# Kernel optimization log

Hardware: AMD Instinct MI355X
Metric: run time of the kernel (lower is better)

## Reference

```python
import jax, jax.numpy as jnp
import numpy as np

EPS = 1e-5  # BatchNorm eps (eval mode, running mean 0 / var 1)
NEG_SLOPE = 0.2


def _knn_idx(x, k):
    # x: [B,C,N] -> idx [B,N,k] (indices of k largest of negative sq dist = k nearest)
    inner = jnp.einsum('bcn,bcm->bnm', x, x)
    xx = jnp.sum(x * x, axis=1)  # [B,N]
    pd = 2.0 * inner - xx[:, :, None] - xx[:, None, :]
    return jax.lax.top_k(pd, k)[1]


def _edge_feature(x, k):
    # x: [B,C,N] -> edge features [B,2C,N,k] = concat(neighbor - center, center)
    idx = _knn_idx(x, k)                        # [B,N,k]
    xt = jnp.transpose(x, (0, 2, 1))            # [B,N,C]
    nbr = jax.vmap(lambda f, i: f[i])(xt, idx)  # [B,N,k,C] gather per batch
    ctr = jnp.broadcast_to(xt[:, :, None, :], nbr.shape)
    feat = jnp.concatenate([nbr - ctr, ctr], axis=-1)  # [B,N,k,2C]
    return jnp.transpose(feat, (0, 3, 1, 2))


def _bn(x, g, b):
    # eval-mode BatchNorm: running_mean=0, running_var=1 -> x * g/sqrt(1+eps) + b
    inv = 1.0 / np.sqrt(1.0 + EPS)
    sh = (1, -1) + (1,) * (x.ndim - 2)
    return x * (g * inv).reshape(sh) + b.reshape(sh)


def _lrelu(x):
    return jnp.where(x >= 0, x, NEG_SLOPE * x)


def _conv2d(x, w, b):  # 1x1 Conv2d: x [B,Ci,N,K], w [Ci,Co]
    return jnp.einsum('bcnk,co->bonk', x, w) + b[None, :, None, None]


def _conv1d(x, w, b):  # 1x1 Conv1d: x [B,Ci,N], w [Ci,Co]
    return jnp.einsum('bcn,co->bon', x, w) + b[None, :, None]


def setup_inputs() -> dict:
    key = jax.random.key(0)
    ks = jax.random.split(key, 24)
    B, N = 8, 4096
    rn = lambda k, sh, s=0.1: (jax.random.normal(k, sh, dtype=jnp.float32) * s)
    inp = {
        'point': jax.random.normal(ks[0], (B, 3, N), dtype=jnp.float32),
        # conv1_1: Conv2d(6,64)
        'w11': rn(ks[1], (6, 64)), 'b11': rn(ks[2], (64,)),
        'g11': jnp.ones((64,), jnp.float32), 'bb11': jnp.zeros((64,), jnp.float32),
        # conv1_2: Conv2d(6,64)
        'w12': rn(ks[3], (6, 64)), 'b12': rn(ks[4], (64,)),
        'g12': jnp.ones((64,), jnp.float32), 'bb12': jnp.zeros((64,), jnp.float32),
        # conv1_3: Conv1d(128,64)
        'w13': rn(ks[5], (128, 64)), 'b13': rn(ks[6], (64,)),
        'g13': jnp.ones((64,), jnp.float32), 'bb13': jnp.zeros((64,), jnp.float32),
        # conv1_5: Conv2d(128,64)
        'w15': rn(ks[7], (128, 64)), 'b15': rn(ks[8], (64,)),
        'g15': jnp.ones((64,), jnp.float32), 'bb15': jnp.zeros((64,), jnp.float32),
        # conv1_4: Conv1d(64,128)
        'w14': rn(ks[9], (64, 128)), 'b14': rn(ks[10], (128,)),
        'g14': jnp.ones((128,), jnp.float32), 'bb14': jnp.zeros((128,), jnp.float32),
        # fc1: Linear(128,64) + ReLU + Linear(64,3)
        'wf1': rn(ks[11], (128, 64)), 'bf1': rn(ks[12], (64,)),
        'wf2': rn(ks[13], (64, 3)), 'bf2': rn(ks[14], (3,)),
    }
    return inp


def reference(point, w11, b11, g11, bb11, w12, b12, g12, bb12,
              w13, b13, g13, bb13, w15, b15, g15, bb15,
              w14, b14, g14, bb14, wf1, bf1, wf2, bf2):
    # point: [B,3,N]
    f = _edge_feature(point, 8)                    # [B,6,N,8]
    f1 = _lrelu(_bn(_conv2d(f, w11, b11), g11, bb11)).max(axis=-1)   # [B,64,N]
    f = _edge_feature(point, 16)                   # [B,6,N,16]
    f2 = _lrelu(_bn(_conv2d(f, w12, b12), g12, bb12)).max(axis=-1)   # [B,64,N]
    f = jnp.concatenate([f1, f2], axis=1)          # [B,128,N]
    f = _lrelu(_bn(_conv1d(f, w13, b13), g13, bb13))                 # [B,64,N]
    g = _edge_feature(f, 16)                       # [B,128,N,16]
    g = _lrelu(_bn(_conv2d(g, w15, b15), g15, bb15)).max(axis=-1)    # [B,64,N]
    g = _lrelu(_bn(_conv1d(g, w14, b14), g14, bb14))                 # [B,128,N]
    feat = jnp.transpose(g, (0, 2, 1))             # [B,N,128]
    h = jax.nn.relu(feat @ wf1 + bf1) @ wf2 + bf2  # [B,N,3]
    refinepoint = h + jnp.transpose(point, (0, 2, 1))
    return feat, refinepoint
```

## Files before the change

### kernel.cpp

```cpp
#include <hip/hip_runtime.h>
#include <math.h>

#define NB 8
#define NP 4096
#define FEAT_SZ (NB * NP * 128)
#define INVBN 0.9999950000374999f
#define SPLIT 2
#define CHUNKS 32

typedef unsigned long long u64;
typedef unsigned int u32;

__device__ __forceinline__ u32 fmap(float f) {
    u32 b = __float_as_uint(f);
    return b ^ ((u32)((int)b >> 31) | 0x80000000u);
}

__device__ __forceinline__ u64 umax64(u64 a, u64 b) { return a > b ? a : b; }

__device__ __forceinline__ void kins(u64 (&v)[16], u64 key) {
    if (key <= v[15]) return;
    bool bb[16];
#pragma unroll
    for (int j = 0; j < 16; ++j) bb[j] = key > v[j];
#pragma unroll
    for (int j = 15; j >= 1; --j) v[j] = bb[j] ? (bb[j - 1] ? v[j - 1] : key) : v[j];
    if (bb[0]) v[0] = key;
}

__device__ __forceinline__ void bufpush(u64 (&v)[16], u64 &q0, u64 &q1, u64 &q2, u64 &q3,
                                        int &cnt, u64 key) {
    if (cnt < 4) {
        q0 = cnt == 0 ? key : q0;
        q1 = cnt == 1 ? key : q1;
        q2 = cnt == 2 ? key : q2;
        q3 = cnt == 3 ? key : q3;
        ++cnt;
    } else {
        kins(v, key);
    }
}

__device__ __forceinline__ void bufflush(u64 (&v)[16], u64 &q0, u64 &q1, u64 &q2, u64 &q3,
                                         int &cnt) {
    kins(v, q0); kins(v, q1); kins(v, q2); kins(v, q3);
    q0 = 0; q1 = 0; q2 = 0; q3 = 0; cnt = 0;
}

__device__ __forceinline__ void bclean(u64 (&v)[16]) {
#pragma unroll
    for (int d = 8; d; d >>= 1) {
#pragma unroll
        for (int i = 0; i < 16; ++i) {
            if ((i & d) == 0) {
                u64 a = v[i], b = v[i | d];
                bool s = a < b;
                v[i] = s ? b : a;
                v[i | d] = s ? a : b;
            }
        }
    }
}

__device__ __forceinline__ void merge_shfl(u64 (&v)[16], int off) {
    u64 o[16];
#pragma unroll
    for (int j = 0; j < 16; ++j) o[j] = __shfl_down(v[j], off);
#pragma unroll
    for (int j = 0; j < 16; ++j) {
        u64 b = o[15 - j];
        v[j] = v[j] > b ? v[j] : b;
    }
    bclean(v);
}

__device__ __forceinline__ u64 rowmax8(u64 x) {
    x = umax64(x, __shfl_xor(x, 1));
    x = umax64(x, __shfl_xor(x, 2));
    x = umax64(x, __shfl_xor(x, 4));
    return x;
}

__global__ __launch_bounds__(256) void knn_point_kernel(const float* __restrict__ point,
                                                        int* __restrict__ idxP) {
    __shared__ float4 pts[NP];
    int bt = blockIdx.x >> 7;
    int n0 = (blockIdx.x & 127) << 5;
    const float* pb = point + (size_t)bt * 3 * NP;
    for (int m = threadIdx.x; m < NP; m += 256) {
        float x = pb[m], y = pb[NP + m], z = pb[2 * NP + m];
        pts[m] = make_float4(x, y, z, fmaf(z, z, fmaf(y, y, x * x)));
    }
    __syncthreads();
    int t = threadIdx.x;
    int q = t & 7;
    float4 c = pts[n0 + (t >> 3)];
    u64 v[16];
#pragma unroll
    for (int j = 0; j < 16; ++j) v[j] = 0;
    u64 b0 = 0, b1 = 0, b2 = 0, b3 = 0;
    int cnt = 0;
    u64 th = 0;
#pragma unroll 1
    for (int o = 0; o < 8; ++o) {
#pragma unroll 4
        for (int ii = 0; ii < 64; ++ii) {
            int m = (((o << 6) + ii) << 3) + q;
            float4 p = pts[m];
            float inner = fmaf(c.z, p.z, fmaf(c.y, p.y, c.x * p.x));
            float pd = fmaf(2.0f, inner, -c.w) - p.w;
            u64 key = ((u64)fmap(pd) << 32) | (u64)(u32)~m;
            if (key > th) bufpush(v, b0, b1, b2, b3, cnt, key);
        }
        if (__any(cnt >= 3)) {
            bufflush(v, b0, b1, b2, b3, cnt);
            th = rowmax8(v[15]);
        }
    }
    bufflush(v, b0, b1, b2, b3, cnt);
    merge_shfl(v, 4);
    merge_shfl(v, 2);
    merge_shfl(v, 1);
    if (q == 0) {
        int* op = idxP + ((size_t)bt * NP + n0 + (t >> 3)) * 16;
#pragma unroll
        for (int j = 0; j < 16; ++j) op[j] = (int)~(u32)v[j];
    }
}

__global__ __launch_bounds__(256) void edge12_kernel(
    const float* __restrict__ point, const int* __restrict__ idxP,
    const float* __restrict__ w11, const float* __restrict__ b11,
    const float* __restrict__ g11, const float* __restrict__ bb11,
    const float* __restrict__ w12, const float* __restrict__ b12,
    const float* __restrict__ g12, const float* __restrict__ bb12,
    float* __restrict__ f12) {
    int lane = threadIdx.x & 63;
    int pt = blockIdx.x * 4 + (threadIdx.x >> 6);
    int bt = pt >> 12, n = pt & (NP - 1);
    const float* pb = point + (size_t)bt * 3 * NP;
    float wd1[3], wc1[3], wd2[3], wc2[3];
#pragma unroll
    for (int c = 0; c < 3; ++c) {
        wd1[c] = w11[c * 64 + lane]; wc1[c] = w11[(3 + c) * 64 + lane];
        wd2[c] = w12[c * 64 + lane]; wc2[c] = w12[(3 + c) * 64 + lane];
    }
    float s1 = g11[lane] * INVBN, sh1 = bb11[lane];
    float s2 = g12[lane] * INVBN, sh2 = bb12[lane];
    float cx = pb[n], cy = pb[NP + n], cz = pb[2 * NP + n];
    float base1 = fmaf(wc1[2], cz, fmaf(wc1[1], cy, fmaf(wc1[0], cx, b11[lane])));
    float base2 = fmaf(wc2[2], cz, fmaf(wc2[1], cy, fmaf(wc2[0], cx, b12[lane])));
    float a1 = -INFINITY, a2 = -INFINITY;
    const int* nb = idxP + (size_t)pt * 16;
#pragma unroll
    for (int j = 0; j < 16; ++j) {
        int m = nb[j];
        float ex = pb[m] - cx, ey = pb[NP + m] - cy, ez = pb[2 * NP + m] - cz;
        float y2 = fmaf(wd2[2], ez, fmaf(wd2[1], ey, fmaf(wd2[0], ex, base2)));
        float z2 = fmaf(y2, s2, sh2);
        z2 = z2 >= 0.f ? z2 : 0.2f * z2;
        a2 = fmaxf(a2, z2);
        if (j < 8) {
            float y1 = fmaf(wd1[2], ez, fmaf(wd1[1], ey, fmaf(wd1[0], ex, base1)));
            float z1 = fmaf(y1, s1, sh1);
            z1 = z1 >= 0.f ? z1 : 0.2f * z1;
            a1 = fmaxf(a1, z1);
        }
    }
    f12[((size_t)pt << 7) + lane] = a1;
    f12[((size_t)pt << 7) + 64 + lane] = a2;
}

template<int K, int O, int MODE, bool XX>
__global__ __launch_bounds__(256) void gemm_act_kernel(
        const float* __restrict__ in, const float* __restrict__ W,
        const float* __restrict__ b, const float* __restrict__ g,
        const float* __restrict__ s, float* __restrict__ outp,
        float* __restrict__ xxo) {
    __shared__ __align__(16) char smem[64 * (K + 1) * 4 + K * O * 4];
    float* A  = (float*)smem;
    float* Wl = (float*)(smem + 64 * (K + 1) * 4);
    float* Hs = (float*)smem;
    constexpr int F4R = K / 4;
#pragma unroll
    for (int i = 0; i < 64 * F4R / 256; ++i) {
        int f = threadIdx.x + i * 256;
        int pt = f / F4R, c4 = f % F4R;
        float4 v = *(const float4*)(in + ((size_t)blockIdx.x * 64 + pt) * K + c4 * 4);
        float* d = A + pt * (K + 1) + c4 * 4;
        d[0] = v.x; d[1] = v.y; d[2] = v.z; d[3] = v.w;
    }
    if constexpr (MODE == 0) {
#pragma unroll
        for (int i = 0; i < 8; ++i) {
            int f = threadIdx.x + i * 256;
            int half = f >= 1024;
            int fr = f & 1023;
            int c = fr >> 4, o4 = fr & 15;
            const float* src = half ? (W + (64 + c) * 64 + o4 * 4) : (W + c * 64 + o4 * 4);
            float4 v = *(const float4*)src;
            float* d = Wl + c * 128 + half * 64 + o4 * 4;
            d[0] = v.x; d[1] = v.y; d[2] = v.z; d[3] = v.w;
        }
    } else {
#pragma unroll
        for (int i = 0; i < K * O / 1024; ++i) {
            int f = threadIdx.x + i * 256;
            *(float4*)(Wl + f * 4) = *(const float4*)(W + f * 4);
        }
    }
    __syncthreads();
    constexpr int NO = O / 8;
    int po = threadIdx.x & 7, pp = threadIdx.x >> 3;
    int pt0 = pp * 2, o0 = po * NO;
    float acc[2][NO];
#pragma unroll
    for (int i = 0; i < NO; ++i) {
        int o = o0 + i;
        float init;
        if constexpr (MODE == 0) init = (o < 64) ? 0.f : b[o - 64];
        else init = b[o];
        acc[0][i] = init;
        acc[1][i] = init;
    }
#pragma unroll 8
    for (int kk = 0; kk < K; ++kk) {
        float a0 = A[pt0 * (K + 1) + kk];
        float a1 = A[(pt0 + 1) * (K + 1) + kk];
        float w[NO];
#pragma unroll
        for (int i4 = 0; i4 < NO / 4; ++i4) {
            float4 wv = *(const float4*)(Wl + kk * O + o0 + i4 * 4);
            w[i4 * 4 + 0] = wv.x; w[i4 * 4 + 1] = wv.y;
            w[i4 * 4 + 2] = wv.z; w[i4 * 4 + 3] = wv.w;
        }
#pragma unroll
        for (int i = 0; i < NO; ++i) {
            acc[0][i] = fmaf(a0, w[i], acc[0][i]);
            acc[1][i] = fmaf(a1, w[i], acc[1][i]);
        }
    }
    float tact[2][NO];
#pragma unroll
    for (int p = 0; p < 2; ++p) {
#pragma unroll
        for (int i = 0; i < NO; ++i) {
            int o = o0 + i;
            float a = acc[p][i];
            if constexpr (MODE == 0) {
                tact[p][i] = a;
            } else {
                float vv = fmaf(a, g[o] * INVBN, s[o]);
                tact[p][i] = vv >= 0.f ? vv : 0.2f * vv;
            }
        }
    }
#pragma unroll
    for (int p = 0; p < 2; ++p) {
        size_t rowg = (size_t)blockIdx.x * 64 + pt0 + p;
#pragma unroll
        for (int i4 = 0; i4 < NO / 4; ++i4) {
            float4 ov;
            ov.x = tact[p][i4 * 4 + 0]; ov.y = tact[p][i4 * 4 + 1];
            ov.z = tact[p][i4 * 4 + 2]; ov.w = tact[p][i4 * 4 + 3];
            *(float4*)(outp + rowg * O + o0 + i4 * 4) = ov;
        }
    }
    if constexpr (XX) {
        __syncthreads();
#pragma unroll
        for (int p = 0; p < 2; ++p)
#pragma unroll
            for (int i = 0; i < NO; ++i)
                Hs[(pt0 + p) * 65 + o0 + i] = tact[p][i];
        __syncthreads();
        if (threadIdx.x < 64) {
            float ss = 0.f;
#pragma unroll
            for (int c = 0; c < 64; ++c) {
                float hc = Hs[threadIdx.x * 65 + c];
                ss = fmaf(hc, hc, ss);
            }
            xxo[(size_t)blockIdx.x * 64 + threadIdx.x] = ss;
        }
    }
}

__global__ __launch_bounds__(256, 2) void knn_feat_kernel(const float* __restrict__ h1t,
                                                          const float* __restrict__ xxf,
                                                          u64* __restrict__ partF) {
    __shared__ __align__(16) char smem[81920];
    float* At = (float*)smem;
    float* Bt = (float*)(smem + 32768);
    u32*   Sb = (u32*)(smem + 49152);
    int seg = blockIdx.x & 1;
    int rg  = (blockIdx.x >> 1) & 31;
    int bt  = blockIdx.x >> 6;
    int n0  = rg << 7;
    int tid = threadIdx.x;
    int rp = tid >> 4;
    int cg = tid & 15;
    int cs = cg << 2;
    const float* hbase = h1t + ((size_t)bt * NP << 6);
    const float* hA = hbase + ((size_t)n0 << 6);
#pragma unroll
    for (int rep = 0; rep < 8; ++rep) {
        int row = rep * 16 + rp;
        float4 va = *(const float4*)(hA + (row << 6) + cs);
        float fv[4] = {va.x, va.y, va.z, va.w};
#pragma unroll
        for (int i = 0; i < 4; ++i) {
            int ch = cs + i;
            int rw = row ^ ((row & 32) >> 3) ^ (((ch >> 2) & 7) << 2);
            At[ch * 128 + rw] = fv[i];
        }
    }
    int m00 = seg * (CHUNKS * 64);
#pragma unroll
    for (int rep = 0; rep < 4; ++rep) {
        int col = rep * 16 + rp;
        float4 vb = *(const float4*)(hbase + ((size_t)(m00 + col) << 6) + cs);
        float fv[4] = {vb.x, vb.y, vb.z, vb.w};
#pragma unroll
        for (int i = 0; i < 4; ++i) {
            int ch = cs + i;
            int cl = col ^ ((col & 32) >> 3) ^ (((ch >> 2) & 7) << 2);
            Bt[ch * 64 + cl] = fv[i];
        }
    }
    float xa[8];
    {
        const float* xap = xxf + bt * NP + n0 + rp * 8;
        float4 t0 = *(const float4*)xap;
        float4 t1 = *(const float4*)(xap + 4);
        xa[0]=t0.x; xa[1]=t0.y; xa[2]=t0.z; xa[3]=t0.w;
        xa[4]=t1.x; xa[5]=t1.y; xa[6]=t1.z; xa[7]=t1.w;
    }
    int r = tid >> 1, h = tid & 1;
    u64 v[16];
#pragma unroll
    for (int j = 0; j < 16; ++j) v[j] = 0;
    u64 q0 = 0, q1 = 0, q2 = 0, q3 = 0;
    int cnt = 0;
    u32 th32 = 0;
    int ab0 = (rp * 8) ^ (rp & 4);
    int ab1 = (rp * 8 + 4) ^ (rp & 4);
    int cb0 = (cg * 4) ^ ((cg & 8) >> 1);
    int swQ = ((r ^ (r >> 3)) & 7) << 2;
    __syncthreads();
#pragma unroll 1
    for (int mcl = 0; mcl < CHUNKS; ++mcl) {
        int m0c = m00 + (mcl << 6);
        bool more = (mcl + 1) < CHUNKS;
        float4 nv0, nv1, nv2, nv3;
        if (more) {
            const float* hn = hbase + ((size_t)(m0c + 64) << 6);
            nv0 = *(const float4*)(hn + ((0 * 16 + rp) << 6) + cs);
            nv1 = *(const float4*)(hn + ((1 * 16 + rp) << 6) + cs);
            nv2 = *(const float4*)(hn + ((2 * 16 + rp) << 6) + cs);
            nv3 = *(const float4*)(hn + ((3 * 16 + rp) << 6) + cs);
        }
        float4 xbv = *(const float4*)(xxf + bt * NP + m0c + (cg << 2));
        float acc[8][4];
#pragma unroll
        for (int i = 0; i < 8; ++i)
#pragma unroll
            for (int j = 0; j < 4; ++j) acc[i][j] = 0.f;
#pragma unroll 1
        for (int gI = 0; gI < 16; ++gI) {
            int sw = (gI & 7) << 2;
            const float* pa0 = At + (gI << 9) + (ab0 ^ sw);
            const float* pa1 = At + (gI << 9) + (ab1 ^ sw);
            const float* pbq = Bt + (gI << 8) + (cb0 ^ sw);
#pragma unroll
            for (int u = 0; u < 4; ++u) {
                float4 a0 = *(const float4*)(pa0 + (u << 7));
                float4 a1 = *(const float4*)(pa1 + (u << 7));
                float4 bq = *(const float4*)(pbq + (u << 6));
                float av[8] = {a0.x, a0.y, a0.z, a0.w, a1.x, a1.y, a1.z, a1.w};
                float bv[4] = {bq.x, bq.y, bq.z, bq.w};
#pragma unroll
                for (int i = 0; i < 8; ++i)
#pragma unroll
                    for (int j = 0; j < 4; ++j)
                        acc[i][j] = fmaf(av[i], bv[j], acc[i][j]);
            }
        }
        float xbs[4] = {xbv.x, xbv.y, xbv.z, xbv.w};
#pragma unroll
        for (int i = 0; i < 8; ++i) {
            int row = rp * 8 + i;
            u32 k0, k1, k2, k3;
            {
                float pd;
                pd = fmaf(2.0f, acc[i][0], -xa[i]) - xbs[0]; k0 = fmap(pd);
                pd = fmaf(2.0f, acc[i][1], -xa[i]) - xbs[1]; k1 = fmap(pd);
                pd = fmaf(2.0f, acc[i][2], -xa[i]) - xbs[2]; k2 = fmap(pd);
                pd = fmaf(2.0f, acc[i][3], -xa[i]) - xbs[3]; k3 = fmap(pd);
            }
            int sq = ((row ^ (row >> 3)) & 7) << 2;
            *(uint4*)(Sb + row * 64 + ((cg << 2) ^ sq)) = make_uint4(k0, k1, k2, k3);
        }
        __syncthreads();
#pragma unroll
        for (int sI = 0; sI < 8; ++sI) {
            int c0 = h * 32 + (sI << 2);
            uint4 kq = *(const uint4*)(Sb + r * 64 + (c0 ^ swQ));
            u32 m01 = kq.x > kq.y ? kq.x : kq.y;
            u32 m23 = kq.z > kq.w ? kq.z : kq.w;
            u32 mx = m01 > m23 ? m01 : m23;
            if (mx >= th32) {
                u32 ks[4] = {kq.x, kq.y, kq.z, kq.w};
#pragma unroll
                for (int j = 0; j < 4; ++j) {
                    if (ks[j] >= th32) {
                        u64 key = ((u64)ks[j] << 32) | (u64)(u32)~(m0c + c0 + j);
                        bufpush(v, q0, q1, q2, q3, cnt, key);
                    }
                }
            }
        }
        if (more) {
            float fva[4][4] = {{nv0.x, nv0.y, nv0.z, nv0.w}, {nv1.x, nv1.y, nv1.z, nv1.w},
                               {nv2.x, nv2.y, nv2.z, nv2.w}, {nv3.x, nv3.y, nv3.z, nv3.w}};
#pragma unroll
            for (int rep = 0; rep < 4; ++rep) {
                int col = rep * 16 + rp;
#pragma unroll
                for (int i = 0; i < 4; ++i) {
                    int ch = cs + i;
                    int cl = col ^ ((col & 32) >> 3) ^ (((ch >> 2) & 7) << 2);
                    Bt[ch * 64 + cl] = fva[rep][i];
                }
            }
        }
        if (__any(cnt >= 3)) {
            bufflush(v, q0, q1, q2, q3, cnt);
            u64 m = umax64(v[15], __shfl_xor(v[15], 1));
            th32 = (u32)(m >> 32);
        }
        __syncthreads();
    }
    bufflush(v, q0, q1, q2, q3, cnt);
    merge_shfl(v, 1);
    if (h == 0) {
        u64* op = partF + (((size_t)bt * NP + n0 + r) * SPLIT + seg) * 16;
#pragma unroll
        for (int j = 0; j < 16; ++j) op[j] = v[j];
    }
}

__global__ __launch_bounds__(256) void edge5_combine_kernel(const float* __restrict__ ZC,
        const u64* __restrict__ partF,
        const float* __restrict__ g15, const float* __restrict__ bb15,
        float* __restrict__ g64t) {
    __shared__ int midx[4][16];
    int lane = threadIdx.x & 63;
    int w = threadIdx.x >> 6;
    int pt = blockIdx.x * 4 + w;
    int bt = pt >> 12;
    if (lane == 0) {
        const u64* base = partF + (size_t)pt * (SPLIT * 16);
        u64 a[16];
#pragma unroll
        for (int j = 0; j < 16; ++j) a[j] = base[j];
#pragma unroll
        for (int j = 0; j < 16; ++j) {
            u64 x = base[16 + (15 - j)];
            a[j] = a[j] > x ? a[j] : x;
        }
        bclean(a);
#pragma unroll
        for (int j = 0; j < 16; ++j) midx[w][j] = (int)~(u32)a[j];
    }
    __syncthreads();
    const float* zrow = ZC + ((size_t)pt << 7);
    float zn = zrow[lane];
    float d = zrow[64 + lane] - zn;
    float sc = g15[lane] * INVBN, sh = bb15[lane];
    const float* zb = ZC + (((size_t)bt * NP) << 7);
    float a = -INFINITY;
    float zm = zb[((size_t)midx[w][0] << 7) + lane];
#pragma unroll 1
    for (int j = 0; j < 16; ++j) {
        float zc = zm;
        if (j < 15) zm = zb[((size_t)midx[w][j + 1] << 7) + lane];
        float y = zc + d;
        float z = fmaf(y, sc, sh);
        z = z >= 0.f ? z : 0.2f * z;
        a = fmaxf(a, z);
    }
    g64t[((size_t)pt << 6) + lane] = a;
}

__global__ __launch_bounds__(256) void fc_head_kernel(const float* __restrict__ feat,
        const float* __restrict__ point,
        const float* __restrict__ wf1, const float* __restrict__ bf1,
        const float* __restrict__ wf2, const float* __restrict__ bf2,
        float* __restrict__ out) {
    __shared__ float A[64 * 129];
    __shared__ float Wl[128 * 64];
    __shared__ float wf2l[192];
    float* R = Wl;
#pragma unroll
    for (int i = 0; i < 8; ++i) {
        int f = threadIdx.x + i * 256;
        int pt = f >> 5, c4 = f & 31;
        float4 v = *(const float4*)(feat + ((size_t)blockIdx.x * 64 + pt) * 128 + c4 * 4);
        float* d = A + pt * 129 + c4 * 4;
        d[0] = v.x; d[1] = v.y; d[2] = v.z; d[3] = v.w;
    }
#pragma unroll
    for (int i = 0; i < 8; ++i) {
        int f = threadIdx.x + i * 256;
        *(float4*)(Wl + f * 4) = *(const float4*)(wf1 + f * 4);
    }
    if (threadIdx.x < 48)
        *(float4*)(wf2l + threadIdx.x * 4) = *(const float4*)(wf2 + threadIdx.x * 4);
    __syncthreads();
    int po = threadIdx.x & 7, pp = threadIdx.x >> 3;
    int pt0 = pp * 2, o0 = po * 8;
    float acc[2][8];
#pragma unroll
    for (int i = 0; i < 8; ++i) { acc[0][i] = bf1[o0 + i]; acc[1][i] = bf1[o0 + i]; }
#pragma unroll 8
    for (int kk = 0; kk < 128; ++kk) {
        float a0 = A[pt0 * 129 + kk];
        float a1 = A[(pt0 + 1) * 129 + kk];
        float w[8];
#pragma unroll
        for (int i4 = 0; i4 < 2; ++i4) {
            float4 wv = *(const float4*)(Wl + kk * 64 + o0 + i4 * 4);
            w[i4 * 4 + 0] = wv.x; w[i4 * 4 + 1] = wv.y;
            w[i4 * 4 + 2] = wv.z; w[i4 * 4 + 3] = wv.w;
        }
#pragma unroll
        for (int i = 0; i < 8; ++i) {
            acc[0][i] = fmaf(a0, w[i], acc[0][i]);
            acc[1][i] = fmaf(a1, w[i], acc[1][i]);
        }
    }
    __syncthreads();
#pragma unroll
    for (int p = 0; p < 2; ++p)
#pragma unroll
        for (int i = 0; i < 8; ++i)
            R[(pt0 + p) * 65 + o0 + i] = fmaxf(acc[p][i], 0.f);
    __syncthreads();
    if (threadIdx.x < 192) {
        int pt = threadIdx.x / 3, dim = threadIdx.x - pt * 3;
        float ssum = 0.f;
#pragma unroll
        for (int c = 0; c < 64; ++c)
            ssum = fmaf(R[pt * 65 + c], wf2l[c * 3 + dim], ssum);
        int ptg = blockIdx.x * 64 + pt;
        int bt = ptg >> 12, n = ptg & (NP - 1);
        float p = point[((size_t)bt * 3 + dim) * NP + n];
        out[(size_t)FEAT_SZ + (size_t)ptg * 3 + dim] = ssum + bf2[dim] + p;
    }
}

extern "C" void kernel_launch(void* const* d_in, const int* in_sizes, int n_in,
                              void* d_out, int out_size, void* d_ws, size_t ws_size,
                              hipStream_t stream) {
    (void)in_sizes; (void)n_in; (void)out_size; (void)ws_size;
    const float* point = (const float*)d_in[0];
    const float* w11 = (const float*)d_in[1];
    const float* b11 = (const float*)d_in[2];
    const float* g11 = (const float*)d_in[3];
    const float* bb11 = (const float*)d_in[4];
    const float* w12 = (const float*)d_in[5];
    const float* b12 = (const float*)d_in[6];
    const float* g12 = (const float*)d_in[7];
    const float* bb12 = (const float*)d_in[8];
    const float* w13 = (const float*)d_in[9];
    const float* b13 = (const float*)d_in[10];
    const float* g13 = (const float*)d_in[11];
    const float* bb13 = (const float*)d_in[12];
    const float* w15 = (const float*)d_in[13];
    const float* b15 = (const float*)d_in[14];
    const float* g15 = (const float*)d_in[15];
    const float* bb15 = (const float*)d_in[16];
    const float* w14 = (const float*)d_in[17];
    const float* b14 = (const float*)d_in[18];
    const float* g14 = (const float*)d_in[19];
    const float* bb14 = (const float*)d_in[20];
    const float* wf1 = (const float*)d_in[21];
    const float* bf1 = (const float*)d_in[22];
    const float* wf2 = (const float*)d_in[23];
    const float* bf2 = (const float*)d_in[24];

    char* ws = (char*)d_ws;
    int*   idxP  = (int*)ws;
    float* xxf   = (float*)(ws + (2u << 20));
    float* h1t   = (float*)(ws + (4u << 20));
    float* g64t  = (float*)(ws + (4u << 20));
    u64*   partF = (u64*)(ws + (12u << 20));
    float* f12   = (float*)(ws + (20u << 20));
    float* ZC    = (float*)(ws + (20u << 20));
    float* feat  = (float*)d_out;

    knn_point_kernel<<<dim3(NB * 128), dim3(256), 0, stream>>>(point, idxP);
    edge12_kernel<<<dim3(NB * NP / 4), dim3(256), 0, stream>>>(
        point, idxP, w11, b11, g11, bb11, w12, b12, g12, bb12, f12);
    gemm_act_kernel<128, 64, 1, true><<<dim3(NB * NP / 64), dim3(256), 0, stream>>>(
        f12, w13, b13, g13, bb13, h1t, xxf);
    knn_feat_kernel<<<dim3(NB * 32 * SPLIT), dim3(256), 0, stream>>>(h1t, xxf, partF);
    gemm_act_kernel<64, 128, 0, false><<<dim3(NB * NP / 64), dim3(256), 0, stream>>>(
        h1t, w15, b15, nullptr, nullptr, ZC, nullptr);
    edge5_combine_kernel<<<dim3(NB * NP / 4), dim3(256), 0, stream>>>(
        ZC, partF, g15, bb15, g64t);
    gemm_act_kernel<64, 128, 1, false><<<dim3(NB * NP / 64), dim3(256), 0, stream>>>(
        g64t, w14, b14, g14, bb14, feat, nullptr);
    fc_head_kernel<<<dim3(NB * NP / 64), dim3(256), 0, stream>>>(
        feat, point, wf1, bf1, wf2, bf2, (float*)d_out);
}
```

Measured before the change: 970.6 us.

## Shrink knn_feat row tile to 64 and fuse edge5 gather with conv14 GEMM

The feature-space kNN kernel now processes 64 query rows per block instead of 128. This halves its shared memory and raises the occupancy hint to 3, and doubles the grid. Only half the threads do top-k selection, which keeps the per-row selection layout. The edge5 gather/max is merged with the following 64->128 conv GEMM into one kernel, so the g64t intermediate no longer goes through global memory and one launch is removed. The trade-off is a lower FMA-per-load ratio in the kNN GEMM and fewer active threads during selection.

```diff
diff --git a/kernel.cpp b/kernel.cpp
--- a/kernel.cpp
+++ b/kernel.cpp
@@ -286,17 +286,17 @@
     }
 }
 
-__global__ __launch_bounds__(256, 2) void knn_feat_kernel(const float* __restrict__ h1t,
+__global__ __launch_bounds__(256, 3) void knn_feat_kernel(const float* __restrict__ h1t,
                                                           const float* __restrict__ xxf,
                                                           u64* __restrict__ partF) {
-    __shared__ __align__(16) char smem[81920];
+    __shared__ __align__(16) char smem[49152];
     float* At = (float*)smem;
-    float* Bt = (float*)(smem + 32768);
-    u32*   Sb = (u32*)(smem + 49152);
+    float* Bt = (float*)(smem + 16384);
+    u32*   Sb = (u32*)(smem + 32768);
     int seg = blockIdx.x & 1;
-    int rg  = (blockIdx.x >> 1) & 31;
-    int bt  = blockIdx.x >> 6;
-    int n0  = rg << 7;
+    int rg  = (blockIdx.x >> 1) & 63;
+    int bt  = blockIdx.x >> 7;
+    int n0  = rg << 6;
     int tid = threadIdx.x;
     int rp = tid >> 4;
     int cg = tid & 15;
@@ -304,7 +304,7 @@
     const float* hbase = h1t + ((size_t)bt * NP << 6);
     const float* hA = hbase + ((size_t)n0 << 6);
 #pragma unroll
-    for (int rep = 0; rep < 8; ++rep) {
+    for (int rep = 0; rep < 4; ++rep) {
         int row = rep * 16 + rp;
         float4 va = *(const float4*)(hA + (row << 6) + cs);
         float fv[4] = {va.x, va.y, va.z, va.w};
@@ -312,7 +312,7 @@
         for (int i = 0; i < 4; ++i) {
             int ch = cs + i;
             int rw = row ^ ((row & 32) >> 3) ^ (((ch >> 2) & 7) << 2);
-            At[ch * 128 + rw] = fv[i];
+            At[ch * 64 + rw] = fv[i];
         }
     }
     int m00 = seg * (CHUNKS * 64);
@@ -328,13 +328,10 @@
             Bt[ch * 64 + cl] = fv[i];
         }
     }
-    float xa[8];
+    float xa[4];
     {
-        const float* xap = xxf + bt * NP + n0 + rp * 8;
-        float4 t0 = *(const float4*)xap;
-        float4 t1 = *(const float4*)(xap + 4);
-        xa[0]=t0.x; xa[1]=t0.y; xa[2]=t0.z; xa[3]=t0.w;
-        xa[4]=t1.x; xa[5]=t1.y; xa[6]=t1.z; xa[7]=t1.w;
+        float4 t0 = *(const float4*)(xxf + bt * NP + n0 + rp * 4);
+        xa[0] = t0.x; xa[1] = t0.y; xa[2] = t0.z; xa[3] = t0.w;
     }
     int r = tid >> 1, h = tid & 1;
     u64 v[16];
@@ -343,9 +340,8 @@
     u64 q0 = 0, q1 = 0, q2 = 0, q3 = 0;
     int cnt = 0;
     u32 th32 = 0;
-    int ab0 = (rp * 8) ^ (rp & 4);
-    int ab1 = (rp * 8 + 4) ^ (rp & 4);
-    int cb0 = (cg * 4) ^ ((cg & 8) >> 1);
+    int ab0 = (rp << 2) ^ ((rp & 8) >> 1);
+    int cb0 = (cg << 2) ^ ((cg & 8) >> 1);
     int swQ = ((r ^ (r >> 3)) & 7) << 2;
     __syncthreads();
 #pragma unroll 1
@@ -361,26 +357,24 @@
             nv3 = *(const float4*)(hn + ((3 * 16 + rp) << 6) + cs);
         }
         float4 xbv = *(const float4*)(xxf + bt * NP + m0c + (cg << 2));
-        float acc[8][4];
-#pragma unroll
-        for (int i = 0; i < 8; ++i)
+        float acc[4][4];
+#pragma unroll
+        for (int i = 0; i < 4; ++i)
 #pragma unroll
             for (int j = 0; j < 4; ++j) acc[i][j] = 0.f;
 #pragma unroll 1
         for (int gI = 0; gI < 16; ++gI) {
             int sw = (gI & 7) << 2;
-            const float* pa0 = At + (gI << 9) + (ab0 ^ sw);
-            const float* pa1 = At + (gI << 9) + (ab1 ^ sw);
+            const float* pa0 = At + (gI << 8) + (ab0 ^ sw);
             const float* pbq = Bt + (gI << 8) + (cb0 ^ sw);
 #pragma unroll
             for (int u = 0; u < 4; ++u) {
-                float4 a0 = *(const float4*)(pa0 + (u << 7));
-                float4 a1 = *(const float4*)(pa1 + (u << 7));
+                float4 a0 = *(const float4*)(pa0 + (u << 6));
                 float4 bq = *(const float4*)(pbq + (u << 6));
-                float av[8] = {a0.x, a0.y, a0.z, a0.w, a1.x, a1.y, a1.z, a1.w};
+                float av[4] = {a0.x, a0.y, a0.z, a0.w};
                 float bv[4] = {bq.x, bq.y, bq.z, bq.w};
 #pragma unroll
-                for (int i = 0; i < 8; ++i)
+                for (int i = 0; i < 4; ++i)
 #pragma unroll
                     for (int j = 0; j < 4; ++j)
                         acc[i][j] = fmaf(av[i], bv[j], acc[i][j]);
@@ -388,8 +382,8 @@
         }
         float xbs[4] = {xbv.x, xbv.y, xbv.z, xbv.w};
 #pragma unroll
-        for (int i = 0; i < 8; ++i) {
-            int row = rp * 8 + i;
+        for (int i = 0; i < 4; ++i) {
+            int row = rp * 4 + i;
             u32 k0, k1, k2, k3;
             {
                 float pd;
@@ -402,22 +396,29 @@
             *(uint4*)(Sb + row * 64 + ((cg << 2) ^ sq)) = make_uint4(k0, k1, k2, k3);
         }
         __syncthreads();
-#pragma unroll
-        for (int sI = 0; sI < 8; ++sI) {
-            int c0 = h * 32 + (sI << 2);
-            uint4 kq = *(const uint4*)(Sb + r * 64 + (c0 ^ swQ));
-            u32 m01 = kq.x > kq.y ? kq.x : kq.y;
-            u32 m23 = kq.z > kq.w ? kq.z : kq.w;
-            u32 mx = m01 > m23 ? m01 : m23;
-            if (mx >= th32) {
-                u32 ks[4] = {kq.x, kq.y, kq.z, kq.w};
-#pragma unroll
-                for (int j = 0; j < 4; ++j) {
-                    if (ks[j] >= th32) {
-                        u64 key = ((u64)ks[j] << 32) | (u64)(u32)~(m0c + c0 + j);
-                        bufpush(v, q0, q1, q2, q3, cnt, key);
+        if (tid < 128) {
+#pragma unroll
+            for (int sI = 0; sI < 8; ++sI) {
+                int c0 = h * 32 + (sI << 2);
+                uint4 kq = *(const uint4*)(Sb + r * 64 + (c0 ^ swQ));
+                u32 m01 = kq.x > kq.y ? kq.x : kq.y;
+                u32 m23 = kq.z > kq.w ? kq.z : kq.w;
+                u32 mx = m01 > m23 ? m01 : m23;
+                if (mx >= th32) {
+                    u32 ks[4] = {kq.x, kq.y, kq.z, kq.w};
+#pragma unroll
+                    for (int j = 0; j < 4; ++j) {
+                        if (ks[j] >= th32) {
+                            u64 key = ((u64)ks[j] << 32) | (u64)(u32)~(m0c + c0 + j);
+                            bufpush(v, q0, q1, q2, q3, cnt, key);
+                        }
                     }
                 }
+            }
+            if (__any(cnt >= 3)) {
+                bufflush(v, q0, q1, q2, q3, cnt);
+                u64 m = umax64(v[15], __shfl_xor(v[15], 1));
+                th32 = (u32)(m >> 32);
             }
         }
         if (more) {
@@ -434,32 +435,36 @@
                 }
             }
         }
-        if (__any(cnt >= 3)) {
-            bufflush(v, q0, q1, q2, q3, cnt);
-            u64 m = umax64(v[15], __shfl_xor(v[15], 1));
-            th32 = (u32)(m >> 32);
-        }
         __syncthreads();
     }
-    bufflush(v, q0, q1, q2, q3, cnt);
-    merge_shfl(v, 1);
-    if (h == 0) {
-        u64* op = partF + (((size_t)bt * NP + n0 + r) * SPLIT + seg) * 16;
-#pragma unroll
-        for (int j = 0; j < 16; ++j) op[j] = v[j];
-    }
-}
-
-__global__ __launch_bounds__(256) void edge5_combine_kernel(const float* __restrict__ ZC,
-        const u64* __restrict__ partF,
+    if (tid < 128) {
+        bufflush(v, q0, q1, q2, q3, cnt);
+        merge_shfl(v, 1);
+        if (h == 0) {
+            u64* op = partF + (((size_t)bt * NP + n0 + r) * SPLIT + seg) * 16;
+#pragma unroll
+            for (int j = 0; j < 16; ++j) op[j] = v[j];
+        }
+    }
+}
+
+__global__ __launch_bounds__(256, 3) void edge5_gemm14_kernel(
+        const float* __restrict__ ZC, const u64* __restrict__ partF,
         const float* __restrict__ g15, const float* __restrict__ bb15,
-        float* __restrict__ g64t) {
-    __shared__ int midx[4][16];
-    int lane = threadIdx.x & 63;
-    int w = threadIdx.x >> 6;
-    int pt = blockIdx.x * 4 + w;
-    int bt = pt >> 12;
-    if (lane == 0) {
+        const float* __restrict__ w14, const float* __restrict__ b14,
+        const float* __restrict__ g14, const float* __restrict__ bb14,
+        float* __restrict__ feat) {
+    __shared__ int midx[64][16];
+    __shared__ float Ag[64 * 65];
+    __shared__ float Wl[64 * 128];
+    int tid = threadIdx.x;
+#pragma unroll
+    for (int i = 0; i < 8; ++i) {
+        int f = tid + i * 256;
+        *(float4*)(Wl + f * 4) = *(const float4*)(w14 + f * 4);
+    }
+    if (tid < 64) {
+        int pt = blockIdx.x * 64 + tid;
         const u64* base = partF + (size_t)pt * (SPLIT * 16);
         u64 a[16];
 #pragma unroll
@@ -471,26 +476,71 @@
         }
         bclean(a);
 #pragma unroll
-        for (int j = 0; j < 16; ++j) midx[w][j] = (int)~(u32)a[j];
-    }
-    __syncthreads();
-    const float* zrow = ZC + ((size_t)pt << 7);
-    float zn = zrow[lane];
-    float d = zrow[64 + lane] - zn;
+        for (int j = 0; j < 16; ++j) midx[tid][j] = (int)~(u32)a[j];
+    }
+    __syncthreads();
+    int lane = tid & 63, w = tid >> 6;
+    int bt = (blockIdx.x * 64) >> 12;
+    const float* zb = ZC + (((size_t)bt * NP) << 7);
     float sc = g15[lane] * INVBN, sh = bb15[lane];
-    const float* zb = ZC + (((size_t)bt * NP) << 7);
-    float a = -INFINITY;
-    float zm = zb[((size_t)midx[w][0] << 7) + lane];
 #pragma unroll 1
-    for (int j = 0; j < 16; ++j) {
-        float zc = zm;
-        if (j < 15) zm = zb[((size_t)midx[w][j + 1] << 7) + lane];
-        float y = zc + d;
-        float z = fmaf(y, sc, sh);
-        z = z >= 0.f ? z : 0.2f * z;
-        a = fmaxf(a, z);
-    }
-    g64t[((size_t)pt << 6) + lane] = a;
+    for (int pp = 0; pp < 16; ++pp) {
+        int p = w * 16 + pp;
+        int pt = blockIdx.x * 64 + p;
+        const float* zrow = ZC + ((size_t)pt << 7);
+        float zn = zrow[lane];
+        float d = zrow[64 + lane] - zn;
+        float zl[16];
+#pragma unroll
+        for (int j = 0; j < 16; ++j)
+            zl[j] = zb[((size_t)midx[p][j] << 7) + lane];
+        float a = -INFINITY;
+#pragma unroll
+        for (int j = 0; j < 16; ++j) {
+            float z = fmaf(zl[j] + d, sc, sh);
+            z = z >= 0.f ? z : 0.2f * z;
+            a = fmaxf(a, z);
+        }
+        Ag[p * 65 + lane] = a;
+    }
+    __syncthreads();
+    int po = tid & 7, pq = tid >> 3;
+    int pt0 = pq * 2, o0 = po * 16;
+    float acc[2][16];
+#pragma unroll
+    for (int i = 0; i < 16; ++i) { acc[0][i] = b14[o0 + i]; acc[1][i] = b14[o0 + i]; }
+#pragma unroll 8
+    for (int kk = 0; kk < 64; ++kk) {
+        float a0 = Ag[pt0 * 65 + kk];
+        float a1 = Ag[(pt0 + 1) * 65 + kk];
+        float wv[16];
+#pragma unroll
+        for (int i4 = 0; i4 < 4; ++i4) {
+            float4 t = *(const float4*)(Wl + kk * 128 + o0 + i4 * 4);
+            wv[i4 * 4 + 0] = t.x; wv[i4 * 4 + 1] = t.y;
+            wv[i4 * 4 + 2] = t.z; wv[i4 * 4 + 3] = t.w;
+        }
+#pragma unroll
+        for (int i = 0; i < 16; ++i) {
+            acc[0][i] = fmaf(a0, wv[i], acc[0][i]);
+            acc[1][i] = fmaf(a1, wv[i], acc[1][i]);
+        }
+    }
+#pragma unroll
+    for (int p = 0; p < 2; ++p) {
+        size_t rowg = (size_t)blockIdx.x * 64 + pt0 + p;
+#pragma unroll
+        for (int i4 = 0; i4 < 4; ++i4) {
+            float4 ov;
+#pragma unroll
+            for (int j = 0; j < 4; ++j) {
+                int o = o0 + i4 * 4 + j;
+                float vv = fmaf(acc[p][i4 * 4 + j], g14[o] * INVBN, bb14[o]);
+                ((float*)&ov)[j] = vv >= 0.f ? vv : 0.2f * vv;
+            }
+            *(float4*)(feat + rowg * 128 + o0 + i4 * 4) = ov;
+        }
+    }
 }
 
 __global__ __launch_bounds__(256) void fc_head_kernel(const float* __restrict__ feat,
@@ -594,7 +644,6 @@
     int*   idxP  = (int*)ws;
     float* xxf   = (float*)(ws + (2u << 20));
     float* h1t   = (float*)(ws + (4u << 20));
-    float* g64t  = (float*)(ws + (4u << 20));
     u64*   partF = (u64*)(ws + (12u << 20));
     float* f12   = (float*)(ws + (20u << 20));
     float* ZC    = (float*)(ws + (20u << 20));
@@ -605,13 +654,11 @@
         point, idxP, w11, b11, g11, bb11, w12, b12, g12, bb12, f12);
     gemm_act_kernel<128, 64, 1, true><<<dim3(NB * NP / 64), dim3(256), 0, stream>>>(
         f12, w13, b13, g13, bb13, h1t, xxf);
-    knn_feat_kernel<<<dim3(NB * 32 * SPLIT), dim3(256), 0, stream>>>(h1t, xxf, partF);
+    knn_feat_kernel<<<dim3(NB * 64 * SPLIT), dim3(256), 0, stream>>>(h1t, xxf, partF);
     gemm_act_kernel<64, 128, 0, false><<<dim3(NB * NP / 64), dim3(256), 0, stream>>>(
         h1t, w15, b15, nullptr, nullptr, ZC, nullptr);
-    edge5_combine_kernel<<<dim3(NB * NP / 4), dim3(256), 0, stream>>>(
-        ZC, partF, g15, bb15, g64t);
-    gemm_act_kernel<64, 128, 1, false><<<dim3(NB * NP / 64), dim3(256), 0, stream>>>(
-        g64t, w14, b14, g14, bb14, feat, nullptr);
+    edge5_gemm14_kernel<<<dim3(NB * NP / 64), dim3(256), 0, stream>>>(
+        ZC, partF, g15, bb15, w14, b14, g14, bb14, feat);
     fc_head_kernel<<<dim3(NB * NP / 64), dim3(256), 0, stream>>>(
         feat, point, wf1, bf1, wf2, bf2, (float*)d_out);
 }
```

Result: slower. 1.123 ms (+15.7%).
